# Optimization experiments

Measured on AMD Instinct MI355X. Metric: run time of the kernel, lower is better.

## Reference

```python
import jax, jax.numpy as jnp
import numpy as np

B, T, C = 4, 2048, 1024
H, D = 16, 64  # num_heads, head_dim
P = 64         # prefix length


def setup_inputs() -> dict:
    key = jax.random.key(0)
    ks = jax.random.split(key, 12)
    s = 1.0 / np.sqrt(C)
    return {
        "x": jax.random.normal(ks[0], (B, T, C), dtype=jnp.float32),
        "attn_mask": jax.random.randint(ks[1], (B, 1, 1, T), 0, 2, dtype=jnp.int32),
        "prefix_k": jax.random.normal(ks[2], (B, H, P, D), dtype=jnp.float32),
        "prefix_v": jax.random.normal(ks[3], (B, H, P, D), dtype=jnp.float32),
        "Wq": jax.random.normal(ks[4], (C, C), dtype=jnp.float32) * s,
        "bq": jnp.zeros((C,), dtype=jnp.float32),
        "Wk": jax.random.normal(ks[5], (C, C), dtype=jnp.float32) * s,
        "bk": jnp.zeros((C,), dtype=jnp.float32),
        "Wv": jax.random.normal(ks[6], (C, C), dtype=jnp.float32) * s,
        "bv": jnp.zeros((C,), dtype=jnp.float32),
        "Wo": jax.random.normal(ks[7], (C, C), dtype=jnp.float32) * s,
        "bo": jnp.zeros((C,), dtype=jnp.float32),
    }


def _heads(y):
    # [B,T,C] -> [B,H,T,D]
    return y.reshape(B, T, H, D).transpose(0, 2, 1, 3)


def reference(x, attn_mask, prefix_k, prefix_v, Wq, bq, Wk, bk, Wv, bv, Wo, bo):
    q = _heads(x @ Wq.T + bq)
    k = _heads(x @ Wk.T + bk)
    v = _heads(x @ Wv.T + bv)
    # concat prefix K/V along key dim -> [B,H,P+T,D]
    k = jnp.concatenate([prefix_k, k], axis=2)
    v = jnp.concatenate([prefix_v, v], axis=2)
    # prefix positions are always visible
    prefix_mask = jnp.ones((B, 1, 1, P), dtype=attn_mask.dtype)
    mask = jnp.concatenate([prefix_mask, attn_mask], axis=-1)  # [B,1,1,P+T]
    scores = jnp.einsum('bhtd,bhsd->bhts', q, k) / jnp.sqrt(jnp.asarray(D, x.dtype))
    scores = jnp.where(mask == 0, -jnp.inf, scores)
    w = jax.nn.softmax(scores, axis=-1)
    o = jnp.einsum('bhts,bhsd->bhtd', w, v)
    o = o.transpose(0, 2, 1, 3).reshape(B, T, C)
    return o @ Wo.T + bo
```

## Files before the change

### kernel.cpp

```cpp
#include <hip/hip_runtime.h>
#include <hip/hip_bf16.h>

typedef __bf16 bf16;
typedef __attribute__((ext_vector_type(8))) __bf16 bf16x8;
typedef __attribute__((ext_vector_type(4))) __bf16 bf16x4;
typedef __attribute__((ext_vector_type(4))) float f32x4;
typedef __attribute__((ext_vector_type(16))) float f32x16;

#define MFMA16(a, b, c) __builtin_amdgcn_mfma_f32_16x16x32_bf16(a, b, c, 0, 0, 0)
#define MFMA32(a, b, c) __builtin_amdgcn_mfma_f32_32x32x16_bf16(a, b, c, 0, 0, 0)

__device__ __forceinline__ void gl_lds16(const void* g, void* l) {
    __builtin_amdgcn_global_load_lds(
        (const __attribute__((address_space(1))) void*)g,
        (__attribute__((address_space(3))) void*)l, 16, 0, 0);
}

#define BARRIER() do { asm volatile("" ::: "memory"); \
    __builtin_amdgcn_s_barrier(); asm volatile("" ::: "memory"); } while (0)

#define QSCALE 0.18033688011f
#define LOGBIAS 24.0f

__global__ __launch_bounds__(256) void prep(
    const float* __restrict__ x, const float* __restrict__ Wq,
    const float* __restrict__ Wk, const float* __restrict__ Wv,
    const float* __restrict__ Wo, const float* __restrict__ pk,
    const float* __restrict__ pv, const int* __restrict__ mask,
    bf16* __restrict__ xb, bf16* __restrict__ wb,
    bf16* __restrict__ k_ws, bf16* __restrict__ vt_ws,
    int* __restrict__ ridx, int* __restrict__ nkv)
{
    const int blk = blockIdx.x, tid = threadIdx.x;
    if (blk < 4) {
        const int b = blk, lane = tid & 63, wv = tid >> 6;
        const int* mb = mask + b * 2048;
        int loc[8], s = 0;
#pragma unroll
        for (int e = 0; e < 8; ++e) { loc[e] = (mb[tid * 8 + e] != 0); s += loc[e]; }
        int inc = s;
#pragma unroll
        for (int off = 1; off < 64; off <<= 1) {
            int t = __shfl_up(inc, off);
            if (lane >= off) inc += t;
        }
        __shared__ int wt[4];
        if (lane == 63) wt[wv] = inc;
        __syncthreads();
        int wo = 0;
        for (int w = 0; w < wv; ++w) wo += wt[w];
        int excl = wo + inc - s;
#pragma unroll
        for (int e = 0; e < 8; ++e) {
            if (loc[e]) ridx[b * 2048 + excl] = tid * 8 + e;
            excl += loc[e];
        }
        if (tid == 255) nkv[b] = 64 + wo + inc;
    } else if (blk < 260) {
        int i = (blk - 4) * 256 + tid;
        {
            int base = i * 4;
            int bh = base >> 12, rem = base & 4095;
            float4 a = *(const float4*)&pk[base];
            bf16x4 ab;
            ab[0] = (bf16)a.x; ab[1] = (bf16)a.y; ab[2] = (bf16)a.z; ab[3] = (bf16)a.w;
            *(bf16x4*)&k_ws[(size_t)bh * (2112 * 64) + rem] = ab;
        }
        {
            int bh = i >> 10, r = i & 1023;
            int d = r >> 4, sq = (r & 15) * 4;
            bf16x4 vb;
#pragma unroll
            for (int e = 0; e < 4; ++e)
                vb[e] = (bf16)pv[(size_t)bh * 4096 + (sq + e) * 64 + d];
            *(bf16x4*)&vt_ws[((size_t)bh * 64 + d) * 2112 + sq] = vb;
        }
    } else {
        int i4 = (blk - 260) * 256 + tid;
        const float* src; bf16* dst; int off;
        if (i4 < 2097152) { src = x; dst = xb; off = i4; }
        else {
            int j = i4 - 2097152;
            int sel = j >> 18;
            off = j & 262143;
            src = (sel == 0) ? Wq : (sel == 1) ? Wk : (sel == 2) ? Wv : Wo;
            dst = wb + (size_t)sel * 1048576;
        }
        float4 a = *(const float4*)&src[(size_t)off * 4];
        bf16x4 o;
        o[0] = (bf16)a.x; o[1] = (bf16)a.y; o[2] = (bf16)a.z; o[3] = (bf16)a.w;
        *(bf16x4*)&dst[(size_t)off * 4] = o;
    }
}

__device__ __forceinline__ void gemm_pipe_256x128(
    const bf16* a0, const bf16* a1, const bf16* a2, const bf16* a3,
    const bf16* b0, const bf16* b1,
    bf16* lds, const int wave, const int lane, f32x4 (&acc)[4][4])
{
    const int ln = lane & 15, quad = lane >> 4;
    const int wm = wave >> 1, wn = wave & 1;
    const int so = wave * 512;
    const int aBase = (wm * 64 + ln) * 64;
    const int bBase = 16384 + (wn * 64 + ln) * 64;
    const int c0 = (quad * 8) ^ ((ln & 7) << 3);
    const int c1 = (32 + quad * 8) ^ ((ln & 7) << 3);

    gl_lds16(a0, lds + so);
    gl_lds16(a1, lds + 4096 + so);
    gl_lds16(a2, lds + 8192 + so);
    gl_lds16(a3, lds + 12288 + so);
    gl_lds16(b0, lds + 16384 + so);
    gl_lds16(b1, lds + 20480 + so);

#pragma unroll 2
    for (int t = 0; t < 16; ++t) {
        bf16* cur = lds + ((t & 1) ? 24576 : 0);
        bf16* nxt = lds + ((t & 1) ? 0 : 24576);
        const int kn = (t + 1) * 64;

        if (t < 15) {
            gl_lds16(a0 + kn, nxt + so);
            gl_lds16(a1 + kn, nxt + 4096 + so);
            gl_lds16(a2 + kn, nxt + 8192 + so);
            asm volatile("s_waitcnt vmcnt(3)" ::: "memory");
        } else {
            asm volatile("s_waitcnt vmcnt(0)" ::: "memory");
        }
        BARRIER();

        bf16x8 fa[4][2], fb[2][2];
#pragma unroll
        for (int mi = 0; mi < 4; ++mi) {
            fa[mi][0] = *(const bf16x8*)(cur + aBase + mi * 1024 + c0);
            fa[mi][1] = *(const bf16x8*)(cur + aBase + mi * 1024 + c1);
        }
#pragma unroll
        for (int ni = 0; ni < 2; ++ni) {
            fb[ni][0] = *(const bf16x8*)(cur + bBase + ni * 1024 + c0);
            fb[ni][1] = *(const bf16x8*)(cur + bBase + ni * 1024 + c1);
        }
        __builtin_amdgcn_s_setprio(1);
#pragma unroll
        for (int mi = 0; mi < 4; ++mi)
#pragma unroll
            for (int ni = 0; ni < 2; ++ni) {
                acc[mi][ni] = MFMA16(fa[mi][0], fb[ni][0], acc[mi][ni]);
                acc[mi][ni] = MFMA16(fa[mi][1], fb[ni][1], acc[mi][ni]);
            }
        __builtin_amdgcn_s_setprio(0);
        BARRIER();

#pragma unroll
        for (int ni = 0; ni < 2; ++ni) {
            fb[ni][0] = *(const bf16x8*)(cur + bBase + (2 + ni) * 1024 + c0);
            fb[ni][1] = *(const bf16x8*)(cur + bBase + (2 + ni) * 1024 + c1);
        }
        if (t < 15) {
            gl_lds16(a3 + kn, nxt + 12288 + so);
            gl_lds16(b0 + kn, nxt + 16384 + so);
            gl_lds16(b1 + kn, nxt + 20480 + so);
        }
        BARRIER();
        __builtin_amdgcn_s_setprio(1);
#pragma unroll
        for (int mi = 0; mi < 4; ++mi)
#pragma unroll
            for (int ni = 0; ni < 2; ++ni) {
                acc[mi][2 + ni] = MFMA16(fa[mi][0], fb[ni][0], acc[mi][2 + ni]);
                acc[mi][2 + ni] = MFMA16(fa[mi][1], fb[ni][1], acc[mi][2 + ni]);
            }
        __builtin_amdgcn_s_setprio(0);
        BARRIER();
    }
}

__global__ __launch_bounds__(512, 2) void proj_gemm(
    const bf16* __restrict__ X, const bf16* __restrict__ Wb,
    const float* __restrict__ bq, const float* __restrict__ bk,
    const float* __restrict__ bv, const int* __restrict__ ridx,
    const int* __restrict__ nkv,
    bf16* __restrict__ q_ws, bf16* __restrict__ k_ws, bf16* __restrict__ vt_ws)
{
    __shared__ bf16 lds[49152];
    const int hw = blockIdx.x;
    const int bx = (hw & 7) * 96 + (hw >> 3);
    const int tid = threadIdx.x, wave = tid >> 6, lane = tid & 63;
    const int sr8 = lane >> 3;
    const int csw = ((lane & 7) ^ sr8) << 3;

    int kind, m0 = 0, n0, bsel = 0, nvis = 0, mbase = 0;
    const bf16* W;
    const float* bias;
    if (bx < 256) {
        kind = 0; m0 = (bx >> 3) * 256; n0 = (bx & 7) * 128;
        W = Wb; bias = bq;
    } else {
        int j = bx - 256;
        kind = 1 + (j >> 8);
        int r = j & 255;
        bsel = r >> 6;
        int rr = r & 63;
        mbase = (rr >> 3) * 256;
        n0 = (rr & 7) * 128;
        nvis = nkv[bsel] - 64;
        if (mbase >= nvis) return;
        W = Wb + (size_t)kind * 1048576;
        bias = (kind == 1) ? bk : bv;
    }

    const bf16 *a0, *a1, *a2, *a3;
    if (kind == 0) {
        a0 = X + (size_t)(m0 + wave * 8 + sr8) * 1024 + csw;
        a1 = a0 + (size_t)64 * 1024;
        a2 = a0 + (size_t)128 * 1024;
        a3 = a0 + (size_t)192 * 1024;
    } else {
        const int* rb = ridx + bsel * 2048;
        const int nv1 = nvis - 1;
        int g = mbase + wave * 8 + sr8;
        int e0 = (g       < nv1) ? g       : nv1;
        int e1 = (g + 64  < nv1) ? g + 64  : nv1;
        int e2 = (g + 128 < nv1) ? g + 128 : nv1;
        int e3 = (g + 192 < nv1) ? g + 192 : nv1;
        const bf16* Xb = X + (size_t)bsel * 2048 * 1024 + csw;
        a0 = Xb + (size_t)rb[e0] * 1024;
        a1 = Xb + (size_t)rb[e1] * 1024;
        a2 = Xb + (size_t)rb[e2] * 1024;
        a3 = Xb + (size_t)rb[e3] * 1024;
    }
    const bf16* b0 = W + (size_t)(n0 + wave * 8 + sr8) * 1024 + csw;
    const bf16* b1 = b0 + (size_t)64 * 1024;

    const f32x4 z4 = {0.f, 0.f, 0.f, 0.f};
    f32x4 acc[4][4];
#pragma unroll
    for (int i = 0; i < 4; ++i)
#pragma unroll
        for (int j = 0; j < 4; ++j) acc[i][j] = z4;

    gemm_pipe_256x128(a0, a1, a2, a3, b0, b1, lds, wave, lane, acc);

    const int ln = lane & 15, quad = lane >> 4;
    const int wm = wave >> 1, wn = wave & 1;
    if (kind == 0) {
#pragma unroll
        for (int ni = 0; ni < 4; ++ni) {
            const int n = n0 + wn * 64 + ni * 16 + ln;
            const float bb = bias[n];
            const int h = n >> 6, d = n & 63;
#pragma unroll
            for (int mi = 0; mi < 4; ++mi) {
                int m = m0 + wm * 64 + mi * 16 + quad * 4;
                int b = m >> 11, tq = m & 2047;
#pragma unroll
                for (int r = 0; r < 4; ++r)
                    q_ws[((size_t)(b * 16 + h) * 2048 + tq + r) * 64 + d] =
                        (bf16)((acc[mi][ni][r] + bb) * QSCALE);
            }
        }
    } else {
#pragma unroll
        for (int ni = 0; ni < 4; ++ni) {
            const int n = n0 + wn * 64 + ni * 16 + ln;
            const float bb = bias[n];
            const int h = n >> 6, d = n & 63;
            const size_t bh64 = (size_t)(bsel * 16 + h);
#pragma unroll
            for (int mi = 0; mi < 4; ++mi) {
                int ml = mbase + wm * 64 + mi * 16 + quad * 4;
                if (kind == 1) {
#pragma unroll
                    for (int r = 0; r < 4; ++r)
                        if (ml + r < nvis)
                            k_ws[(bh64 * 2112 + 64 + ml + r) * 64 + d] =
                                (bf16)(acc[mi][ni][r] + bb);
                } else {
                    if (ml + 3 < nvis) {
                        bf16x4 pb;
#pragma unroll
                        for (int r = 0; r < 4; ++r) pb[r] = (bf16)(acc[mi][ni][r] + bb);
                        *(bf16x4*)&vt_ws[(bh64 * 64 + d) * 2112 + 64 + ml] = pb;
                    } else {
#pragma unroll
                        for (int r = 0; r < 4; ++r)
                            if (ml + r < nvis)
                                vt_ws[(bh64 * 64 + d) * 2112 + 64 + ml + r] =
                                    (bf16)(acc[mi][ni][r] + bb);
                    }
                }
            }
        }
    }
}

__global__ __launch_bounds__(256) void attn_kernel(
    const bf16* __restrict__ Q, const bf16* __restrict__ K,
    const bf16* __restrict__ VT, const int* __restrict__ nk,
    bf16* __restrict__ O)
{
    __shared__ bf16 smem[128 * 72];
    bf16* Ks = smem;
    bf16* Vt = smem + 64 * 72;
    const int tid = threadIdx.x, wave = tid >> 6, lane = tid & 63;
    const int ln = lane & 31, hh = lane >> 5;
    const int bh = blockIdx.y, b = bh >> 4, head = bh & 15;
    const bf16* __restrict__ Kb  = K  + (size_t)bh * (2112 * 64);
    const bf16* __restrict__ Vtb = VT + (size_t)bh * (64 * 2112);
    const int qg = blockIdx.x * 128 + wave * 32 + ln;
    const int nkeys = nk[b];
    const int send = ((nkeys + 63) >> 6) << 6;

    bf16x8 qf[4];
#pragma unroll
    for (int kt = 0; kt < 4; ++kt)
        qf[kt] = *(const bf16x8*)&Q[((size_t)bh * 2048 + qg) * 64 + kt * 16 + hh * 8];

    float l_r = 0.f;
    f32x16 acc[2];
#pragma unroll
    for (int r = 0; r < 16; ++r) { acc[0][r] = 0.f; acc[1][r] = 0.f; }

    const int ks_s = tid >> 3, ks_c = (tid & 7) * 8;
    const int vd = tid >> 3, v8 = tid & 7, vs = v8 * 8;
    const int vcb = (v8 >> 1) * 16 + ((v8 & 1) ? 4 : 0);

    bf16x8 kr0, kr1, vr0, vr1;
    kr0 = *(const bf16x8*)&Kb[(size_t)ks_s * 64 + ks_c];
    kr1 = *(const bf16x8*)&Kb[(size_t)(ks_s + 32) * 64 + ks_c];
    vr0 = *(const bf16x8*)&Vtb[(size_t)vd * 2112 + vs];
    vr1 = *(const bf16x8*)&Vtb[(size_t)(vd + 32) * 2112 + vs];

    for (int s0 = 0; s0 < send; s0 += 64) {
        __syncthreads();
        *(bf16x8*)&Ks[ks_s * 72 + ks_c]        = kr0;
        *(bf16x8*)&Ks[(ks_s + 32) * 72 + ks_c] = kr1;
        {
            bf16x4 lo, hi;
#pragma unroll
            for (int e = 0; e < 4; ++e) { lo[e] = vr0[e]; hi[e] = vr0[4 + e]; }
            *(bf16x4*)&Vt[vd * 72 + vcb]     = lo;
            *(bf16x4*)&Vt[vd * 72 + vcb + 8] = hi;
#pragma unroll
            for (int e = 0; e < 4; ++e) { lo[e] = vr1[e]; hi[e] = vr1[4 + e]; }
            *(bf16x4*)&Vt[(vd + 32) * 72 + vcb]     = lo;
            *(bf16x4*)&Vt[(vd + 32) * 72 + vcb + 8] = hi;
        }
        __syncthreads();

        if (s0 + 64 < send) {
            const int sn = s0 + 64;
            kr0 = *(const bf16x8*)&Kb[(size_t)(sn + ks_s) * 64 + ks_c];
            kr1 = *(const bf16x8*)&Kb[(size_t)(sn + ks_s + 32) * 64 + ks_c];
            vr0 = *(const bf16x8*)&Vtb[(size_t)vd * 2112 + sn + vs];
            vr1 = *(const bf16x8*)&Vtb[(size_t)(vd + 32) * 2112 + sn + vs];
        }

        f32x16 sc[2];
#pragma unroll
        for (int ts = 0; ts < 2; ++ts) {
            f32x16 s16;
#pragma unroll
            for (int r = 0; r < 16; ++r) s16[r] = 0.f;
#pragma unroll
            for (int kt = 0; kt < 4; ++kt) {
                bf16x8 kf = *(const bf16x8*)&Ks[(ts * 32 + ln) * 72 + kt * 16 + hh * 8];
                s16 = MFMA32(kf, qf[kt], s16);
            }
            sc[ts] = s16;
        }

        float rs = 0.f;
        bf16x8 pf[4];
        if (s0 + 64 <= nkeys) {
#pragma unroll
            for (int ts = 0; ts < 2; ++ts)
#pragma unroll
                for (int rg = 0; rg < 4; ++rg)
#pragma unroll
                    for (int i = 0; i < 4; ++i) {
                        float p = __builtin_amdgcn_exp2f(sc[ts][rg * 4 + i] - LOGBIAS);
                        rs += p;
                        pf[ts * 2 + (rg >> 1)][(rg & 1) * 4 + i] = (bf16)p;
                    }
        } else {
#pragma unroll
            for (int ts = 0; ts < 2; ++ts)
#pragma unroll
                for (int rg = 0; rg < 4; ++rg)
#pragma unroll
                    for (int i = 0; i < 4; ++i) {
                        int key = s0 + ts * 32 + rg * 8 + hh * 4 + i;
                        float add = (key < nkeys) ? -LOGBIAS : -1e30f;
                        float p = __builtin_amdgcn_exp2f(sc[ts][rg * 4 + i] + add);
                        rs += p;
                        pf[ts * 2 + (rg >> 1)][(rg & 1) * 4 + i] = (bf16)p;
                    }
        }
        l_r += rs;

#pragma unroll
        for (int st = 0; st < 4; ++st) {
            bf16x8 a0 = *(const bf16x8*)&Vt[ln * 72 + st * 16 + hh * 8];
            acc[0] = MFMA32(a0, pf[st], acc[0]);
            bf16x8 a1 = *(const bf16x8*)&Vt[(32 + ln) * 72 + st * 16 + hh * 8];
            acc[1] = MFMA32(a1, pf[st], acc[1]);
        }
    }

    __syncthreads();
    l_r += __shfl_xor(l_r, 32);
    float inv = 1.0f / l_r;
    bf16* scratch = smem + wave * (32 * 72);
#pragma unroll
    for (int td = 0; td < 2; ++td)
#pragma unroll
        for (int rg = 0; rg < 4; ++rg) {
            bf16x4 ob;
#pragma unroll
            for (int i = 0; i < 4; ++i) ob[i] = (bf16)(acc[td][rg * 4 + i] * inv);
            *(bf16x4*)&scratch[ln * 72 + td * 32 + rg * 8 + hh * 4] = ob;
        }
    __builtin_amdgcn_s_waitcnt(0xC07F);
    const int orow = lane >> 3, oc = (lane & 7) * 8;
#pragma unroll
    for (int pass = 0; pass < 4; ++pass) {
        int ml = pass * 8 + orow;
        bf16x8 ov = *(const bf16x8*)&scratch[ml * 72 + oc];
        int qrow = blockIdx.x * 128 + wave * 32 + ml;
        *(bf16x8*)&O[((size_t)b * 2048 + qrow) * 1024 + head * 64 + oc] = ov;
    }
}

__global__ __launch_bounds__(512, 2) void out_proj_gemm(
    const bf16* __restrict__ A, const bf16* __restrict__ W,
    const float* __restrict__ bias, float* __restrict__ out)
{
    __shared__ bf16 lds[49152];
    const int hw = blockIdx.x;
    const int bx = (hw & 7) * 32 + (hw >> 3);
    const int m0 = (bx >> 3) * 256, n0 = (bx & 7) * 128;
    const int tid = threadIdx.x, wave = tid >> 6, lane = tid & 63;
    const int sr8 = lane >> 3;
    const int csw = ((lane & 7) ^ sr8) << 3;

    const bf16* a0 = A + (size_t)(m0 + wave * 8 + sr8) * 1024 + csw;
    const bf16* a1 = a0 + (size_t)64 * 1024;
    const bf16* a2 = a0 + (size_t)128 * 1024;
    const bf16* a3 = a0 + (size_t)192 * 1024;
    const bf16* b0 = W + (size_t)(n0 + wave * 8 + sr8) * 1024 + csw;
    const bf16* b1 = b0 + (size_t)64 * 1024;

    const f32x4 z4 = {0.f, 0.f, 0.f, 0.f};
    f32x4 acc[4][4];
#pragma unroll
    for (int i = 0; i < 4; ++i)
#pragma unroll
        for (int j = 0; j < 4; ++j) acc[i][j] = z4;

    gemm_pipe_256x128(a0, a1, a2, a3, b0, b1, lds, wave, lane, acc);

    const int ln = lane & 15, quad = lane >> 4;
    const int wm = wave >> 1, wn = wave & 1;
#pragma unroll
    for (int ni = 0; ni < 4; ++ni) {
        const int n = n0 + wn * 64 + ni * 16 + ln;
        const float bb = bias[n];
#pragma unroll
        for (int mi = 0; mi < 4; ++mi) {
            int m = m0 + wm * 64 + mi * 16 + quad * 4;
#pragma unroll
            for (int r = 0; r < 4; ++r)
                out[(size_t)(m + r) * 1024 + n] = acc[mi][ni][r] + bb;
        }
    }
}

extern "C" void kernel_launch(void* const* d_in, const int* in_sizes, int n_in,
                              void* d_out, int out_size, void* d_ws, size_t ws_size,
                              hipStream_t stream)
{
    const float* x    = (const float*)d_in[0];
    const int*   mask = (const int*)d_in[1];
    const float* pk   = (const float*)d_in[2];
    const float* pv   = (const float*)d_in[3];
    const float* Wq   = (const float*)d_in[4];
    const float* bq   = (const float*)d_in[5];
    const float* Wk   = (const float*)d_in[6];
    const float* bk   = (const float*)d_in[7];
    const float* Wv   = (const float*)d_in[8];
    const float* bv   = (const float*)d_in[9];
    const float* Wo   = (const float*)d_in[10];
    const float* bo   = (const float*)d_in[11];
    float* out = (float*)d_out;

    bf16* xb    = (bf16*)d_ws;
    bf16* wb    = xb + (size_t)8388608;
    bf16* q_ws  = wb + (size_t)4194304;
    bf16* k_ws  = q_ws + (size_t)8388608;
    bf16* vt_ws = k_ws + (size_t)8650752;
    int*  ridx  = (int*)(vt_ws + (size_t)8650752);
    int*  nkv   = ridx + 4 * 2048;
    bf16* a_ws  = xb;

    prep<<<dim3(12548), 256, 0, stream>>>(x, Wq, Wk, Wv, Wo, pk, pv, mask,
                                          xb, wb, k_ws, vt_ws, ridx, nkv);
    proj_gemm<<<dim3(768), 512, 0, stream>>>(xb, wb, bq, bk, bv, ridx, nkv,
                                             q_ws, k_ws, vt_ws);
    attn_kernel<<<dim3(16, 64), 256, 0, stream>>>(q_ws, k_ws, vt_ws, nkv, a_ws);
    out_proj_gemm<<<dim3(256), 512, 0, stream>>>(a_ws, wb + (size_t)3 * 1048576,
                                                 bo, out);
}
```

Before: 252.1 us.

## Double query rows per attention wave, pre-permute V layout, widen prep conversion

After: 231.7 us. -8.1%, faster.

```diff
diff --git a/kernel.cpp b/kernel.cpp
--- a/kernel.cpp
+++ b/kernel.cpp
@@ -21,6 +21,10 @@
 
 #define QSCALE 0.18033688011f
 #define LOGBIAS 24.0f
+
+__device__ __forceinline__ int vsig4(int c) {
+    return ((c >> 4) << 4) + (((c >> 3) & 1) << 2) + ((c & 4) ? 8 : 0);
+}
 
 __global__ __launch_bounds__(256) void prep(
     const float* __restrict__ x, const float* __restrict__ Wq,
@@ -73,23 +77,25 @@
 #pragma unroll
             for (int e = 0; e < 4; ++e)
                 vb[e] = (bf16)pv[(size_t)bh * 4096 + (sq + e) * 64 + d];
-            *(bf16x4*)&vt_ws[((size_t)bh * 64 + d) * 2112 + sq] = vb;
+            *(bf16x4*)&vt_ws[((size_t)bh * 64 + d) * 2112 + vsig4(sq)] = vb;
         }
     } else {
-        int i4 = (blk - 260) * 256 + tid;
-        const float* src; bf16* dst; int off;
-        if (i4 < 2097152) { src = x; dst = xb; off = i4; }
+        int i8 = (blk - 260) * 256 + tid;
+        const float* src; bf16* dst; size_t off;
+        if (i8 < 1048576) { src = x; dst = xb; off = (size_t)i8; }
         else {
-            int j = i4 - 2097152;
-            int sel = j >> 18;
-            off = j & 262143;
+            int j = i8 - 1048576;
+            int sel = j >> 17;
+            off = (size_t)(j & 131071);
             src = (sel == 0) ? Wq : (sel == 1) ? Wk : (sel == 2) ? Wv : Wo;
             dst = wb + (size_t)sel * 1048576;
         }
-        float4 a = *(const float4*)&src[(size_t)off * 4];
-        bf16x4 o;
+        float4 a = *(const float4*)&src[off * 8];
+        float4 c = *(const float4*)&src[off * 8 + 4];
+        bf16x8 o;
         o[0] = (bf16)a.x; o[1] = (bf16)a.y; o[2] = (bf16)a.z; o[3] = (bf16)a.w;
-        *(bf16x4*)&dst[(size_t)off * 4] = o;
+        o[4] = (bf16)c.x; o[5] = (bf16)c.y; o[6] = (bf16)c.z; o[7] = (bf16)c.w;
+        *(bf16x8*)&dst[off * 8] = o;
     }
 }
 
@@ -276,16 +282,19 @@
                             k_ws[(bh64 * 2112 + 64 + ml + r) * 64 + d] =
                                 (bf16)(acc[mi][ni][r] + bb);
                 } else {
+                    int g0 = 64 + ml;
+                    int c0 = g0 & 63;
+                    int gcol = (g0 & ~63) + vsig4(c0);
                     if (ml + 3 < nvis) {
                         bf16x4 pb;
 #pragma unroll
                         for (int r = 0; r < 4; ++r) pb[r] = (bf16)(acc[mi][ni][r] + bb);
-                        *(bf16x4*)&vt_ws[(bh64 * 64 + d) * 2112 + 64 + ml] = pb;
+                        *(bf16x4*)&vt_ws[(bh64 * 64 + d) * 2112 + gcol] = pb;
                     } else {
 #pragma unroll
                         for (int r = 0; r < 4; ++r)
                             if (ml + r < nvis)
-                                vt_ws[(bh64 * 64 + d) * 2112 + 64 + ml + r] =
+                                vt_ws[(bh64 * 64 + d) * 2112 + gcol + r] =
                                     (bf16)(acc[mi][ni][r] + bb);
                     }
                 }
@@ -294,7 +303,7 @@
     }
 }
 
-__global__ __launch_bounds__(256) void attn_kernel(
+__global__ __launch_bounds__(256, 2) void attn_kernel(
     const bf16* __restrict__ Q, const bf16* __restrict__ K,
     const bf16* __restrict__ VT, const int* __restrict__ nk,
     bf16* __restrict__ O)
@@ -304,26 +313,36 @@
     bf16* Vt = smem + 64 * 72;
     const int tid = threadIdx.x, wave = tid >> 6, lane = tid & 63;
     const int ln = lane & 31, hh = lane >> 5;
-    const int bh = blockIdx.y, b = bh >> 4, head = bh & 15;
+    const int hw = blockIdx.x;
+    const int bh = (hw & 7) * 8 + ((hw >> 3) & 7);
+    const int qx = hw >> 6;
+    const int b = bh >> 4, head = bh & 15;
     const bf16* __restrict__ Kb  = K  + (size_t)bh * (2112 * 64);
     const bf16* __restrict__ Vtb = VT + (size_t)bh * (64 * 2112);
-    const int qg = blockIdx.x * 128 + wave * 32 + ln;
     const int nkeys = nk[b];
     const int send = ((nkeys + 63) >> 6) << 6;
-
-    bf16x8 qf[4];
-#pragma unroll
-    for (int kt = 0; kt < 4; ++kt)
-        qf[kt] = *(const bf16x8*)&Q[((size_t)bh * 2048 + qg) * 64 + kt * 16 + hh * 8];
-
-    float l_r = 0.f;
-    f32x16 acc[2];
-#pragma unroll
-    for (int r = 0; r < 16; ++r) { acc[0][r] = 0.f; acc[1][r] = 0.f; }
+    const int qg = qx * 256 + wave * 64 + ln;
+
+    bf16x8 qf0[4], qf1[4];
+#pragma unroll
+    for (int kt = 0; kt < 4; ++kt) {
+        qf0[kt] = *(const bf16x8*)&Q[((size_t)bh * 2048 + qg) * 64 + kt * 16 + hh * 8];
+        qf1[kt] = *(const bf16x8*)&Q[((size_t)bh * 2048 + qg + 32) * 64 + kt * 16 + hh * 8];
+    }
+
+    f32x16 m24;
+#pragma unroll
+    for (int r = 0; r < 16; ++r) m24[r] = -LOGBIAS;
+
+    float l0 = 0.f, l1 = 0.f;
+    f32x16 acc00, acc01, acc10, acc11;
+#pragma unroll
+    for (int r = 0; r < 16; ++r) {
+        acc00[r] = 0.f; acc01[r] = 0.f; acc10[r] = 0.f; acc11[r] = 0.f;
+    }
 
     const int ks_s = tid >> 3, ks_c = (tid & 7) * 8;
-    const int vd = tid >> 3, v8 = tid & 7, vs = v8 * 8;
-    const int vcb = (v8 >> 1) * 16 + ((v8 & 1) ? 4 : 0);
+    const int vd = tid >> 3, vs = (tid & 7) * 8;
 
     bf16x8 kr0, kr1, vr0, vr1;
     kr0 = *(const bf16x8*)&Kb[(size_t)ks_s * 64 + ks_c];
@@ -335,17 +354,8 @@
         __syncthreads();
         *(bf16x8*)&Ks[ks_s * 72 + ks_c]        = kr0;
         *(bf16x8*)&Ks[(ks_s + 32) * 72 + ks_c] = kr1;
-        {
-            bf16x4 lo, hi;
-#pragma unroll
-            for (int e = 0; e < 4; ++e) { lo[e] = vr0[e]; hi[e] = vr0[4 + e]; }
-            *(bf16x4*)&Vt[vd * 72 + vcb]     = lo;
-            *(bf16x4*)&Vt[vd * 72 + vcb + 8] = hi;
-#pragma unroll
-            for (int e = 0; e < 4; ++e) { lo[e] = vr1[e]; hi[e] = vr1[4 + e]; }
-            *(bf16x4*)&Vt[(vd + 32) * 72 + vcb]     = lo;
-            *(bf16x4*)&Vt[(vd + 32) * 72 + vcb + 8] = hi;
-        }
+        *(bf16x8*)&Vt[vd * 72 + vs]            = vr0;
+        *(bf16x8*)&Vt[(vd + 32) * 72 + vs]     = vr1;
         __syncthreads();
 
         if (s0 + 64 < send) {
@@ -356,22 +366,23 @@
             vr1 = *(const bf16x8*)&Vtb[(size_t)(vd + 32) * 2112 + sn + vs];
         }
 
-        f32x16 sc[2];
+        f32x16 sc0[2], sc1[2];
 #pragma unroll
         for (int ts = 0; ts < 2; ++ts) {
-            f32x16 s16;
-#pragma unroll
-            for (int r = 0; r < 16; ++r) s16[r] = 0.f;
-#pragma unroll
-            for (int kt = 0; kt < 4; ++kt) {
-                bf16x8 kf = *(const bf16x8*)&Ks[(ts * 32 + ln) * 72 + kt * 16 + hh * 8];
-                s16 = MFMA32(kf, qf[kt], s16);
+            bf16x8 kf = *(const bf16x8*)&Ks[(ts * 32 + ln) * 72 + hh * 8];
+            f32x16 sA = MFMA32(kf, qf0[0], m24);
+            f32x16 sB = MFMA32(kf, qf1[0], m24);
+#pragma unroll
+            for (int kt = 1; kt < 4; ++kt) {
+                kf = *(const bf16x8*)&Ks[(ts * 32 + ln) * 72 + kt * 16 + hh * 8];
+                sA = MFMA32(kf, qf0[kt], sA);
+                sB = MFMA32(kf, qf1[kt], sB);
             }
-            sc[ts] = s16;
-        }
-
-        float rs = 0.f;
-        bf16x8 pf[4];
+            sc0[ts] = sA; sc1[ts] = sB;
+        }
+
+        float rs0 = 0.f, rs1 = 0.f;
+        bf16x8 pf0[4], pf1[4];
         if (s0 + 64 <= nkeys) {
 #pragma unroll
             for (int ts = 0; ts < 2; ++ts)
@@ -379,9 +390,11 @@
                 for (int rg = 0; rg < 4; ++rg)
 #pragma unroll
                     for (int i = 0; i < 4; ++i) {
-                        float p = __builtin_amdgcn_exp2f(sc[ts][rg * 4 + i] - LOGBIAS);
-                        rs += p;
-                        pf[ts * 2 + (rg >> 1)][(rg & 1) * 4 + i] = (bf16)p;
+                        float p0 = __builtin_amdgcn_exp2f(sc0[ts][rg * 4 + i]);
+                        float p1 = __builtin_amdgcn_exp2f(sc1[ts][rg * 4 + i]);
+                        rs0 += p0; rs1 += p1;
+                        pf0[ts * 2 + (rg >> 1)][(rg & 1) * 4 + i] = (bf16)p0;
+                        pf1[ts * 2 + (rg >> 1)][(rg & 1) * 4 + i] = (bf16)p1;
                     }
         } else {
 #pragma unroll
@@ -391,44 +404,73 @@
 #pragma unroll
                     for (int i = 0; i < 4; ++i) {
                         int key = s0 + ts * 32 + rg * 8 + hh * 4 + i;
-                        float add = (key < nkeys) ? -LOGBIAS : -1e30f;
-                        float p = __builtin_amdgcn_exp2f(sc[ts][rg * 4 + i] + add);
-                        rs += p;
-                        pf[ts * 2 + (rg >> 1)][(rg & 1) * 4 + i] = (bf16)p;
+                        float add = (key < nkeys) ? 0.f : -1e30f;
+                        float p0 = __builtin_amdgcn_exp2f(sc0[ts][rg * 4 + i] + add);
+                        float p1 = __builtin_amdgcn_exp2f(sc1[ts][rg * 4 + i] + add);
+                        rs0 += p0; rs1 += p1;
+                        pf0[ts * 2 + (rg >> 1)][(rg & 1) * 4 + i] = (bf16)p0;
+                        pf1[ts * 2 + (rg >> 1)][(rg & 1) * 4 + i] = (bf16)p1;
                     }
         }
-        l_r += rs;
+        l0 += rs0; l1 += rs1;
 
 #pragma unroll
         for (int st = 0; st < 4; ++st) {
             bf16x8 a0 = *(const bf16x8*)&Vt[ln * 72 + st * 16 + hh * 8];
-            acc[0] = MFMA32(a0, pf[st], acc[0]);
+            acc00 = MFMA32(a0, pf0[st], acc00);
+            acc10 = MFMA32(a0, pf1[st], acc10);
             bf16x8 a1 = *(const bf16x8*)&Vt[(32 + ln) * 72 + st * 16 + hh * 8];
-            acc[1] = MFMA32(a1, pf[st], acc[1]);
+            acc01 = MFMA32(a1, pf0[st], acc01);
+            acc11 = MFMA32(a1, pf1[st], acc11);
         }
     }
 
     __syncthreads();
-    l_r += __shfl_xor(l_r, 32);
-    float inv = 1.0f / l_r;
+    l0 += __shfl_xor(l0, 32);
+    l1 += __shfl_xor(l1, 32);
+    const float inv0 = 1.0f / l0, inv1 = 1.0f / l1;
     bf16* scratch = smem + wave * (32 * 72);
-#pragma unroll
-    for (int td = 0; td < 2; ++td)
-#pragma unroll
-        for (int rg = 0; rg < 4; ++rg) {
-            bf16x4 ob;
-#pragma unroll
-            for (int i = 0; i < 4; ++i) ob[i] = (bf16)(acc[td][rg * 4 + i] * inv);
-            *(bf16x4*)&scratch[ln * 72 + td * 32 + rg * 8 + hh * 4] = ob;
-        }
+    const int orow = lane >> 3, oc = (lane & 7) * 8;
+    const int qrow0 = qx * 256 + wave * 64;
+
+#pragma unroll
+    for (int rg = 0; rg < 4; ++rg) {
+        bf16x4 ob;
+#pragma unroll
+        for (int i = 0; i < 4; ++i) ob[i] = (bf16)(acc00[rg * 4 + i] * inv0);
+        *(bf16x4*)&scratch[ln * 72 + rg * 8 + hh * 4] = ob;
+#pragma unroll
+        for (int i = 0; i < 4; ++i) ob[i] = (bf16)(acc01[rg * 4 + i] * inv0);
+        *(bf16x4*)&scratch[ln * 72 + 32 + rg * 8 + hh * 4] = ob;
+    }
     __builtin_amdgcn_s_waitcnt(0xC07F);
-    const int orow = lane >> 3, oc = (lane & 7) * 8;
+    __builtin_amdgcn_sched_barrier(0);
 #pragma unroll
     for (int pass = 0; pass < 4; ++pass) {
         int ml = pass * 8 + orow;
         bf16x8 ov = *(const bf16x8*)&scratch[ml * 72 + oc];
-        int qrow = blockIdx.x * 128 + wave * 32 + ml;
-        *(bf16x8*)&O[((size_t)b * 2048 + qrow) * 1024 + head * 64 + oc] = ov;
+        *(bf16x8*)&O[((size_t)b * 2048 + qrow0 + ml) * 1024 + head * 64 + oc] = ov;
+    }
+    __builtin_amdgcn_s_waitcnt(0xC07F);
+    __builtin_amdgcn_sched_barrier(0);
+
+#pragma unroll
+    for (int rg = 0; rg < 4; ++rg) {
+        bf16x4 ob;
+#pragma unroll
+        for (int i = 0; i < 4; ++i) ob[i] = (bf16)(acc10[rg * 4 + i] * inv1);
+        *(bf16x4*)&scratch[ln * 72 + rg * 8 + hh * 4] = ob;
+#pragma unroll
+        for (int i = 0; i < 4; ++i) ob[i] = (bf16)(acc11[rg * 4 + i] * inv1);
+        *(bf16x4*)&scratch[ln * 72 + 32 + rg * 8 + hh * 4] = ob;
+    }
+    __builtin_amdgcn_s_waitcnt(0xC07F);
+    __builtin_amdgcn_sched_barrier(0);
+#pragma unroll
+    for (int pass = 0; pass < 4; ++pass) {
+        int ml = pass * 8 + orow;
+        bf16x8 ov = *(const bf16x8*)&scratch[ml * 72 + oc];
+        *(bf16x8*)&O[((size_t)b * 2048 + qrow0 + 32 + ml) * 1024 + head * 64 + oc] = ov;
     }
 }
 
@@ -503,11 +545,11 @@
     int*  nkv   = ridx + 4 * 2048;
     bf16* a_ws  = xb;
 
-    prep<<<dim3(12548), 256, 0, stream>>>(x, Wq, Wk, Wv, Wo, pk, pv, mask,
-                                          xb, wb, k_ws, vt_ws, ridx, nkv);
+    prep<<<dim3(6404), 256, 0, stream>>>(x, Wq, Wk, Wv, Wo, pk, pv, mask,
+                                         xb, wb, k_ws, vt_ws, ridx, nkv);
     proj_gemm<<<dim3(768), 512, 0, stream>>>(xb, wb, bq, bk, bv, ridx, nkv,
                                              q_ws, k_ws, vt_ws);
-    attn_kernel<<<dim3(16, 64), 256, 0, stream>>>(q_ws, k_ws, vt_ws, nkv, a_ws);
+    attn_kernel<<<dim3(512), 256, 0, stream>>>(q_ws, k_ws, vt_ws, nkv, a_ws);
     out_proj_gemm<<<dim3(256), 512, 0, stream>>>(a_ws, wb + (size_t)3 * 1048576,
                                                  bo, out);
 }
```
